# Optimization experiments

Measured on AMD Instinct MI355X. Metric: run time of the kernel, lower is better.

Reference implementation:

```python
import jax, jax.numpy as jnp
import numpy as np

BIG_NEG = -1000000000.0
B, N, X, D = 16, 32, 36, 2048
H = 512

def setup_inputs() -> dict:
    key = jax.random.key(0)
    ks = jax.random.split(key, 16)
    inp = {
        'fc_feats_target': jax.random.normal(ks[0], (B, 1, D), jnp.float32),
        'fc_feats_distr': jax.random.normal(ks[1], (B, N, D), jnp.float32),
        'att_feats_target': jax.random.normal(ks[2], (B, 1, X, D), jnp.float32),
        'att_feats_distr': jax.random.normal(ks[3], (B, N, X, D), jnp.float32),
        'att_masks_target': jax.random.randint(ks[4], (B, 1, X), 0, 2, jnp.int32),
        'att_masks_distr': jax.random.randint(ks[5], (B, N, X), 0, 2, jnp.int32),
        # scorer MLP params: Linear(2D->H), Linear(H->1)
        'W1': jax.random.normal(ks[6], (2 * D, H), jnp.float32) * 0.02,
        'b1': jnp.zeros((H,), jnp.float32),
        'W2': jax.random.normal(ks[7], (H, 1), jnp.float32) * 0.02,
        'b2': jnp.zeros((1,), jnp.float32),
        # bilinear weight, initialized to identity as in the module
        'Wbil': jnp.eye(D, dtype=jnp.float32),
        # object_scorer MLP params
        'oW1': jax.random.normal(ks[8], (2 * D, H), jnp.float32) * 0.02,
        'ob1': jnp.zeros((H,), jnp.float32),
        'oW2': jax.random.normal(ks[9], (H, 1), jnp.float32) * 0.02,
        'ob2': jnp.zeros((1,), jnp.float32),
    }
    return inp

def _mlp(x, W1, b1, W2, b2):
    h = jax.nn.relu(x @ W1 + b1)
    return (h @ W2 + b2)[..., 0]  # squeeze(-1)

def reference(fc_feats_target, fc_feats_distr, att_feats_target, att_feats_distr,
              att_masks_target, att_masks_distr,
              W1, b1, W2, b2, Wbil, oW1, ob1, oW2, ob2):
    # base scorer on global (fc) features
    ft = jnp.broadcast_to(fc_feats_target, fc_feats_distr.shape)  # [B,N,D]
    cat_feats = jnp.concatenate([ft, fc_feats_distr], axis=-1)    # [B,N,2D]
    scores = _mlp(cat_feats, W1, b1, W2, b2)                      # [B,N]

    # bilinear compatibility: einsum('bixd,biye,de->bixy') with target broadcast over i
    tproj = jnp.einsum('bxd,de->bxe', att_feats_target[:, 0], Wbil)        # [B,X,D]
    inners = jnp.einsum('bxd,biyd->bixy', tproj, att_feats_distr)          # [B,N,X,Y]

    mask_outer = (att_masks_target[:, 0][:, None, :, None]
                  * att_masks_distr[:, :, None, :])                        # [B,N,X,Y]
    inners = jnp.where(mask_outer > 0, inners, BIG_NEG)

    target_weights = jax.nn.softmax(jnp.max(inners, axis=3), axis=-1)      # [B,N,X]
    distr_weights = jax.nn.softmax(jnp.max(inners, axis=2), axis=-1)       # [B,N,Y]

    target_feats = jnp.einsum('bxd,bix->bid', att_feats_target[:, 0], target_weights)
    distr_feats = jnp.einsum('biyd,biy->bid', att_feats_distr, distr_weights)

    cat_att = jnp.concatenate([target_feats, distr_feats], axis=-1)        # [B,N,2D]
    scores = scores + _mlp(cat_att, oW1, ob1, oW2, ob2)

    return jax.nn.log_softmax(scores, axis=-1)  # [B,N]
```

## Files before the change

### kernel.cpp

```cpp
#include <hip/hip_runtime.h>
#include <math.h>

#define D_   2048
#define H_   512
#define K2D  4096
#define X_   36
#define NCOL 1152

#define Z_MLP 32
#define Z_TP  8

#define O_A   0u
#define O_B   9437184u
#define O_SB  11534336u
#define O_SO  11534848u
#define O_C   11536384u

typedef __attribute__((ext_vector_type(8))) short bf8_t;
typedef __attribute__((ext_vector_type(4))) float f4_t;

__device__ __forceinline__ unsigned short f2bf(float f) {
  unsigned u = __float_as_uint(f);
  unsigned r = u + 0x7FFFu + ((u >> 16) & 1u);
  return (unsigned short)(r >> 16);
}
__device__ __forceinline__ float bf2f(unsigned short h) {
  return __uint_as_float(((unsigned)h) << 16);
}

__device__ __forceinline__ void gload16(const void* g, void* l) {
  __builtin_amdgcn_global_load_lds(
      (const __attribute__((address_space(1))) unsigned int*)g,
      (__attribute__((address_space(3))) unsigned int*)l, 16, 0, 0);
}

#define TSTR 40

__device__ __forceinline__ void cvt8(unsigned short* Hp, unsigned short* Lp,
                                     float4 a, float4 b) {
  __align__(16) unsigned short h[8], l[8];
  float x[8] = {a.x, a.y, a.z, a.w, b.x, b.y, b.z, b.w};
  #pragma unroll
  for (int j = 0; j < 8; j++) {
    h[j] = f2bf(x[j]);
    l[j] = f2bf(x[j] - bf2f(h[j]));
  }
  *(bf8_t*)Hp = *(bf8_t*)&h[0];
  *(bf8_t*)Lp = *(bf8_t*)&l[0];
}

__device__ __forceinline__ void cvt8v(bf8_t* H, bf8_t* L, float4 a, float4 b) {
  float x[8] = {a.x, a.y, a.z, a.w, b.x, b.y, b.z, b.w};
  bf8_t hh, ll;
  #pragma unroll
  for (int j = 0; j < 8; j++) {
    unsigned short h = f2bf(x[j]);
    hh[j] = (short)h;
    ll[j] = (short)f2bf(x[j] - bf2f(h));
  }
  *H = hh; *L = ll;
}

__global__ __launch_bounds__(256, 4) void gemm_mfma64(
    const float* __restrict__ A, const float* __restrict__ A2,
    const float* __restrict__ Bm, float* __restrict__ Cpart,
    int M, int N, int K, int kchunk, int amode)
{
  __shared__ __align__(16) unsigned short AsH[64 * TSTR], AsL[64 * TSTR];
  __shared__ __align__(16) unsigned short BsH[64 * TSTR], BsL[64 * TSTR];
  const int t  = threadIdx.x;
  const int m0 = blockIdx.y << 6;
  const int n0 = blockIdx.x << 6;
  const int k0 = blockIdx.z * kchunk;
  const int kend = k0 + kchunk;
  const int w  = t >> 6;
  const int ln = t & 15;
  const int qd = (t >> 4) & 3;
  const int wm = (w >> 1) << 5;
  const int wn = (w & 1) << 5;
  const int a_row = t >> 2;
  const int a_kq  = (t & 3) << 3;
  const int b_col = t & 63;
  const int b_kq  = (t >> 6) << 3;

  f4_t acc[2][2];
  #pragma unroll
  for (int i = 0; i < 2; i++)
    #pragma unroll
    for (int j = 0; j < 2; j++) acc[i][j] = (f4_t)0.f;

  float4 pa0, pa1;
  float  pb[8];

  auto loadA = [&](int kb) {
    int gr = m0 + a_row;
    int gk = kb + a_kq;
    pa0 = make_float4(0.f, 0.f, 0.f, 0.f);
    pa1 = pa0;
    if (gr < M) {
      const float* src;
      if (amode == 0) src = A + (size_t)gr * K + gk;
      else src = (gk < 2048) ? (A  + ((size_t)(gr >> 5) << 11) + gk)
                             : (A2 + ((size_t)gr << 11) + (gk - 2048));
      pa0 = *(const float4*)src;
      pa1 = *(const float4*)(src + 4);
    }
  };
  auto loadB = [&](int kb) {
    #pragma unroll
    for (int j = 0; j < 8; j++)
      pb[j] = Bm[(size_t)(kb + b_kq + j) * N + n0 + b_col];
  };

  loadA(k0); loadB(k0);

  for (int kb = k0; kb < kend; kb += 32) {
    __syncthreads();
    cvt8(&AsH[a_row * TSTR + a_kq], &AsL[a_row * TSTR + a_kq], pa0, pa1);
    cvt8(&BsH[b_col * TSTR + b_kq], &BsL[b_col * TSTR + b_kq],
         make_float4(pb[0], pb[1], pb[2], pb[3]),
         make_float4(pb[4], pb[5], pb[6], pb[7]));
    __syncthreads();
    if (kb + 32 < kend) { loadA(kb + 32); loadB(kb + 32); }
    bf8_t ah[2], al[2], bh[2], bl[2];
    #pragma unroll
    for (int fm = 0; fm < 2; fm++) {
      int r = (wm + (fm << 4) + ln) * TSTR + (qd << 3);
      ah[fm] = *(const bf8_t*)&AsH[r];
      al[fm] = *(const bf8_t*)&AsL[r];
    }
    #pragma unroll
    for (int fn = 0; fn < 2; fn++) {
      int r = (wn + (fn << 4) + ln) * TSTR + (qd << 3);
      bh[fn] = *(const bf8_t*)&BsH[r];
      bl[fn] = *(const bf8_t*)&BsL[r];
    }
    #pragma unroll
    for (int fm = 0; fm < 2; fm++)
      #pragma unroll
      for (int fn = 0; fn < 2; fn++) {
        acc[fm][fn] = __builtin_amdgcn_mfma_f32_16x16x32_bf16(ah[fm], bh[fn], acc[fm][fn], 0, 0, 0);
        acc[fm][fn] = __builtin_amdgcn_mfma_f32_16x16x32_bf16(ah[fm], bl[fn], acc[fm][fn], 0, 0, 0);
        acc[fm][fn] = __builtin_amdgcn_mfma_f32_16x16x32_bf16(al[fm], bh[fn], acc[fm][fn], 0, 0, 0);
      }
  }
  float* Cz = Cpart + (size_t)blockIdx.z * M * N;
  #pragma unroll
  for (int fm = 0; fm < 2; fm++) {
    #pragma unroll
    for (int reg = 0; reg < 4; reg++) {
      int gr = m0 + wm + (fm << 4) + (qd << 2) + reg;
      if (gr < M) {
        #pragma unroll
        for (int fn = 0; fn < 2; fn++)
          Cz[(size_t)gr * N + n0 + wn + (fn << 4) + ln] = acc[fm][fn][reg];
      }
    }
  }
}

__global__ __launch_bounds__(256) void reduce_tp(
    const float* __restrict__ tpp, unsigned short* __restrict__ tH,
    unsigned short* __restrict__ tL)
{
  int idx = blockIdx.x * 256 + threadIdx.x;
  const float4* p = (const float4*)tpp;
  float4 a = p[idx];
  #pragma unroll
  for (int z = 1; z < Z_TP; z++) {
    float4 b = p[idx + (size_t)z * 294912];
    a.x += b.x; a.y += b.y; a.z += b.z; a.w += b.w;
  }
  ushort4 h, l;
  h.x = f2bf(a.x); l.x = f2bf(a.x - bf2f(h.x));
  h.y = f2bf(a.y); l.y = f2bf(a.y - bf2f(h.y));
  h.z = f2bf(a.z); l.z = f2bf(a.z - bf2f(h.z));
  h.w = f2bf(a.w); l.w = f2bf(a.w - bf2f(h.w));
  ((ushort4*)tH)[idx] = h;
  ((ushort4*)tL)[idx] = l;
}

__global__ __launch_bounds__(256) void mlp_tail_z(
    const float* __restrict__ hp, const float* __restrict__ b1,
    const float* __restrict__ w2, const float* __restrict__ b2,
    float* __restrict__ out)
{
  int row = blockIdx.x;
  int t   = threadIdx.x;
  float v = 0.f;
  #pragma unroll
  for (int q = 0; q < 2; q++) {
    int h = t + (q << 8);
    float s = 0.f;
    #pragma unroll
    for (int z = 0; z < Z_MLP; z++)
      s += hp[(size_t)z * (H_ * 512) + (size_t)row * H_ + h];
    s += b1[h];
    v += fmaxf(s, 0.f) * w2[h];
  }
  #pragma unroll
  for (int off = 32; off > 0; off >>= 1) v += __shfl_down(v, off, 64);
  __shared__ float red[4];
  if ((t & 63) == 0) red[t >> 6] = v;
  __syncthreads();
  if (t == 0) out[row] = red[0] + red[1] + red[2] + red[3] + b2[0];
}

__global__ __launch_bounds__(256, 2) void attn_bi(
    const unsigned short* __restrict__ tH,
    const float* __restrict__ attd,
    const int* __restrict__ amt, const int* __restrict__ amd,
    const float* __restrict__ attt, float* __restrict__ cat)
{
  __shared__ float Sp[4][36][37];
  __shared__ __align__(16) float Bs[4][2][1280];
  __shared__ int   mtv[36], mdv[36];
  __shared__ float mrow[36], mcol[36], twl[36], dwl[36];
  const int bi = blockIdx.x;
  const int b  = bi >> 5;
  const int t  = threadIdx.x;
  const int w  = t >> 6;
  const int lane = t & 63;
  const int ln = t & 15;
  const int qd = (t >> 4) & 3;
  if (t < 36) { mtv[t] = amt[b * 36 + t]; mdv[t] = amd[bi * 36 + t]; }

  const unsigned short* tLo = tH + 1179648;
  const int kw = w << 9;
  const unsigned short* AH[3];
  const unsigned short* AL[3];
  #pragma unroll
  for (int f = 0; f < 3; f++) {
    int r = f * 16 + ln; if (r > 35) r = 35;
    size_t ao = ((size_t)b * X_ + r) * D_ + kw + (qd << 3);
    AH[f] = tH  + ao;
    AL[f] = tLo + ao;
  }
  const float* Bbase = attd + (size_t)bi * X_ * D_;

  f4_t acc[3][3];
  #pragma unroll
  for (int i = 0; i < 3; i++)
    #pragma unroll
    for (int j = 0; j < 3; j++) acc[i][j] = (f4_t)0.f;

  auto stage = [&](int kk, int cc) {
    const int k0 = kw + (kk << 5);
    #pragma unroll
    for (int j = 0; j < 5; j++) {
      int r = j * 8 + (lane >> 3); if (r > 35) r = 35;
      int ss = (lane & 7) ^ (r & 7);
      gload16(Bbase + (size_t)r * D_ + k0 + (ss << 2), &Bs[w][cc][j << 8]);
    }
  };

  bf8_t ah[3], al[3];
  stage(0, 0);
  #pragma unroll
  for (int f = 0; f < 3; f++) {
    ah[f] = *(const bf8_t*)AH[f];
    al[f] = *(const bf8_t*)AL[f];
  }
  asm volatile("s_waitcnt vmcnt(0)" ::: "memory");
  __builtin_amdgcn_sched_barrier(0);

  int c = 0;
  for (int kk = 0; kk < 16; kk++) {
    if (kk < 15) stage(kk + 1, c ^ 1);
    bf8_t anH[3], anL[3];
    if (kk < 15) {
      const int o1 = (kk + 1) << 5;
      #pragma unroll
      for (int f = 0; f < 3; f++) {
        anH[f] = *(const bf8_t*)(AH[f] + o1);
        anL[f] = *(const bf8_t*)(AL[f] + o1);
      }
    }
    #pragma unroll
    for (int fn = 0; fn < 3; fn++) {
      int r = fn * 16 + ln; if (r > 35) r = 35;
      int base = r << 5;
      int s0 = (((qd << 1)    ) ^ (r & 7)) << 2;
      int s1 = (((qd << 1) | 1) ^ (r & 7)) << 2;
      float4 x0 = *(const float4*)&Bs[w][c][base + s0];
      float4 x1 = *(const float4*)&Bs[w][c][base + s1];
      bf8_t bh, bl;
      cvt8v(&bh, &bl, x0, x1);
      #pragma unroll
      for (int fm = 0; fm < 3; fm++) {
        acc[fm][fn] = __builtin_amdgcn_mfma_f32_16x16x32_bf16(ah[fm], bh, acc[fm][fn], 0, 0, 0);
        acc[fm][fn] = __builtin_amdgcn_mfma_f32_16x16x32_bf16(ah[fm], bl, acc[fm][fn], 0, 0, 0);
        acc[fm][fn] = __builtin_amdgcn_mfma_f32_16x16x32_bf16(al[fm], bh, acc[fm][fn], 0, 0, 0);
      }
    }
    asm volatile("s_waitcnt vmcnt(0)" ::: "memory");
    __builtin_amdgcn_sched_barrier(0);
    c ^= 1;
    if (kk < 15) {
      #pragma unroll
      for (int f = 0; f < 3; f++) { ah[f] = anH[f]; al[f] = anL[f]; }
    }
  }

  #pragma unroll
  for (int fm = 0; fm < 3; fm++)
    #pragma unroll
    for (int fn = 0; fn < 3; fn++)
      #pragma unroll
      for (int reg = 0; reg < 4; reg++) {
        int x = (fm << 4) + (qd << 2) + reg;
        int y = (fn << 4) + ln;
        if (x < 36 && y < 36) Sp[w][x][y] = acc[fm][fn][reg];
      }
  __syncthreads();
  for (int e = t; e < 1296; e += 256) {
    int x = e / 36, y = e - x * 36;
    float v = Sp[0][x][y] + Sp[1][x][y] + Sp[2][x][y] + Sp[3][x][y];
    Sp[0][x][y] = (mtv[x] != 0 && mdv[y] != 0) ? v : -1e9f;
  }
  __syncthreads();
  if (t < 36) {
    float r = -INFINITY, c2 = -INFINITY;
    for (int k = 0; k < 36; k++) {
      r  = fmaxf(r,  Sp[0][t][k]);
      c2 = fmaxf(c2, Sp[0][k][t]);
    }
    mrow[t] = r; mcol[t] = c2;
  }
  __syncthreads();
  if (t < 64) {
    float v = (t < 36) ? mrow[t] : -INFINITY;
    float m = v;
    #pragma unroll
    for (int off = 32; off > 0; off >>= 1) m = fmaxf(m, __shfl_xor(m, off, 64));
    float e = (t < 36) ? expf(v - m) : 0.f;
    float s = e;
    #pragma unroll
    for (int off = 32; off > 0; off >>= 1) s += __shfl_xor(s, off, 64);
    if (t < 36) twl[t] = e / s;
  } else if (t < 128) {
    int l = t - 64;
    float v = (l < 36) ? mcol[l] : -INFINITY;
    float m = v;
    #pragma unroll
    for (int off = 32; off > 0; off >>= 1) m = fmaxf(m, __shfl_xor(m, off, 64));
    float e = (l < 36) ? expf(v - m) : 0.f;
    float s = e;
    #pragma unroll
    for (int off = 32; off > 0; off >>= 1) s += __shfl_xor(s, off, 64);
    if (l < 36) dwl[l] = e / s;
  }
  __syncthreads();
  const float4* at4 = (const float4*)(attt + (size_t)b * X_ * D_);
  const float4* ad4 = (const float4*)(attd + (size_t)bi * X_ * D_);
  float4 t0 = make_float4(0, 0, 0, 0), t1 = t0, d0 = t0, d1 = t0;
  for (int x = 0; x < 36; x++) {
    float wt = twl[x], wd = dwl[x];
    float4 a  = at4[x * 512 + t];
    float4 a2 = at4[x * 512 + t + 256];
    float4 e  = ad4[x * 512 + t];
    float4 e2 = ad4[x * 512 + t + 256];
    t0.x = fmaf(wt, a.x, t0.x);  t0.y = fmaf(wt, a.y, t0.y);
    t0.z = fmaf(wt, a.z, t0.z);  t0.w = fmaf(wt, a.w, t0.w);
    t1.x = fmaf(wt, a2.x, t1.x); t1.y = fmaf(wt, a2.y, t1.y);
    t1.z = fmaf(wt, a2.z, t1.z); t1.w = fmaf(wt, a2.w, t1.w);
    d0.x = fmaf(wd, e.x, d0.x);  d0.y = fmaf(wd, e.y, d0.y);
    d0.z = fmaf(wd, e.z, d0.z);  d0.w = fmaf(wd, e.w, d0.w);
    d1.x = fmaf(wd, e2.x, d1.x); d1.y = fmaf(wd, e2.y, d1.y);
    d1.z = fmaf(wd, e2.z, d1.z); d1.w = fmaf(wd, e2.w, d1.w);
  }
  float4* c4 = (float4*)(cat + (size_t)bi * K2D);
  c4[t] = t0; c4[t + 256] = t1; c4[512 + t] = d0; c4[512 + t + 256] = d1;
}

__global__ __launch_bounds__(64) void lsm(
    const float* __restrict__ sb, const float* __restrict__ so,
    float* __restrict__ out)
{
  int b = blockIdx.x, t = threadIdx.x;
  float s = (t < 32) ? sb[b * 32 + t] + so[b * 32 + t] : -INFINITY;
  float m = s;
  #pragma unroll
  for (int off = 32; off > 0; off >>= 1) m = fmaxf(m, __shfl_xor(m, off, 64));
  float e = (t < 32) ? expf(s - m) : 0.f;
  float sum = e;
  #pragma unroll
  for (int off = 32; off > 0; off >>= 1) sum += __shfl_xor(sum, off, 64);
  if (t < 32) out[b * 32 + t] = s - m - logf(sum);
}

extern "C" void kernel_launch(void* const* d_in, const int* in_sizes, int n_in,
                              void* d_out, int out_size, void* d_ws, size_t ws_size,
                              hipStream_t stream)
{
  const float* fc_t  = (const float*)d_in[0];
  const float* fc_d  = (const float*)d_in[1];
  const float* att_t = (const float*)d_in[2];
  const float* att_d = (const float*)d_in[3];
  const int*   am_t  = (const int*)d_in[4];
  const int*   am_d  = (const int*)d_in[5];
  const float* W1    = (const float*)d_in[6];
  const float* b1    = (const float*)d_in[7];
  const float* W2    = (const float*)d_in[8];
  const float* b2    = (const float*)d_in[9];
  const float* Wbil  = (const float*)d_in[10];
  const float* oW1   = (const float*)d_in[11];
  const float* ob1   = (const float*)d_in[12];
  const float* oW2   = (const float*)d_in[13];
  const float* ob2   = (const float*)d_in[14];
  float* ws  = (float*)d_ws;
  float* out = (float*)d_out;

  gemm_mfma64<<<dim3(8, 8, Z_MLP), 256, 0, stream>>>(fc_t, fc_d, W1, ws + O_A,
                                                     512, 512, 4096, 4096 / Z_MLP, 1);
  mlp_tail_z<<<512, 256, 0, stream>>>(ws + O_A, b1, W2, b2, ws + O_SB);
  gemm_mfma64<<<dim3(32, 9, Z_TP), 256, 0, stream>>>(att_t, nullptr, Wbil, ws + O_A,
                                                     576, 2048, 2048, 2048 / Z_TP, 0);
  reduce_tp<<<1152, 256, 0, stream>>>(ws + O_A, (unsigned short*)(ws + O_B),
                                      (unsigned short*)(ws + O_B) + 1179648);
  attn_bi<<<512, 256, 0, stream>>>((const unsigned short*)(ws + O_B), att_d,
                                   am_t, am_d, att_t, ws + O_C);
  gemm_mfma64<<<dim3(8, 8, Z_MLP), 256, 0, stream>>>(ws + O_C, nullptr, oW1, ws + O_A,
                                                     512, 512, 4096, 4096 / Z_MLP, 0);
  mlp_tail_z<<<512, 256, 0, stream>>>(ws + O_A, ob1, oW2, ob2, ws + O_SO);
  lsm<<<16, 64, 0, stream>>>(ws + O_SB, ws + O_SO, out);
}
```

Baseline: 378.9 us.

## Stage shared 128-wide K chunks across all warps in attn_bi bilinear GEMM

Before, each of the four wavefronts staged its own contiguous 512-element K slice of the distractor features into a private LDS buffer. Now the block cooperatively loads 128-column K chunks covering all 36 rows into one shared double buffer, with each wave owning a 32-column sub-slice, and uses a 32-way XOR swizzle. The aim is longer contiguous global reads per row (512 bytes instead of 128) for better coalescing. In exchange it adds a __syncthreads per iteration in place of the wave-local schedule barrier, which serialises the waves.

```diff
diff --git a/kernel.cpp b/kernel.cpp
--- a/kernel.cpp
+++ b/kernel.cpp
@@ -213,7 +213,7 @@
     const float* __restrict__ attt, float* __restrict__ cat)
 {
   __shared__ float Sp[4][36][37];
-  __shared__ __align__(16) float Bs[4][2][1280];
+  __shared__ __align__(16) float Bs[2][36 * 128];
   __shared__ int   mtv[36], mdv[36];
   __shared__ float mrow[36], mcol[36], twl[36], dwl[36];
   const int bi = blockIdx.x;
@@ -226,13 +226,12 @@
   if (t < 36) { mtv[t] = amt[b * 36 + t]; mdv[t] = amd[bi * 36 + t]; }
 
   const unsigned short* tLo = tH + 1179648;
-  const int kw = w << 9;
   const unsigned short* AH[3];
   const unsigned short* AL[3];
   #pragma unroll
   for (int f = 0; f < 3; f++) {
     int r = f * 16 + ln; if (r > 35) r = 35;
-    size_t ao = ((size_t)b * X_ + r) * D_ + kw + (qd << 3);
+    size_t ao = ((size_t)b * X_ + r) * D_ + (w << 5) + (qd << 3);
     AH[f] = tH  + ao;
     AL[f] = tLo + ao;
   }
@@ -244,13 +243,19 @@
     #pragma unroll
     for (int j = 0; j < 3; j++) acc[i][j] = (f4_t)0.f;
 
-  auto stage = [&](int kk, int cc) {
-    const int k0 = kw + (kk << 5);
+  const int g0 = (w < 2) ? w * 5 : 10 + (w - 2) * 4;
+  const int gn = (w < 2) ? 5 : 4;
+  auto stage = [&](int sc, int cc) {
     #pragma unroll
     for (int j = 0; j < 5; j++) {
-      int r = j * 8 + (lane >> 3); if (r > 35) r = 35;
-      int ss = (lane & 7) ^ (r & 7);
-      gload16(Bbase + (size_t)r * D_ + k0 + (ss << 2), &Bs[w][cc][j << 8]);
+      if (j < gn) {
+        int g = g0 + j;
+        int r = (g << 1) + (lane >> 5);
+        int p = lane & 31;
+        int s = p ^ (r & 31);
+        gload16(Bbase + (size_t)r * D_ + (sc << 7) + (s << 2),
+                &Bs[cc][g << 8]);
+      }
     }
   };
 
@@ -262,14 +267,14 @@
     al[f] = *(const bf8_t*)AL[f];
   }
   asm volatile("s_waitcnt vmcnt(0)" ::: "memory");
-  __builtin_amdgcn_sched_barrier(0);
+  __syncthreads();
 
   int c = 0;
-  for (int kk = 0; kk < 16; kk++) {
-    if (kk < 15) stage(kk + 1, c ^ 1);
+  for (int sc = 0; sc < 16; sc++) {
+    if (sc < 15) stage(sc + 1, c ^ 1);
     bf8_t anH[3], anL[3];
-    if (kk < 15) {
-      const int o1 = (kk + 1) << 5;
+    if (sc < 15) {
+      const int o1 = (sc + 1) << 7;
       #pragma unroll
       for (int f = 0; f < 3; f++) {
         anH[f] = *(const bf8_t*)(AH[f] + o1);
@@ -279,11 +284,11 @@
     #pragma unroll
     for (int fn = 0; fn < 3; fn++) {
       int r = fn * 16 + ln; if (r > 35) r = 35;
-      int base = r << 5;
-      int s0 = (((qd << 1)    ) ^ (r & 7)) << 2;
-      int s1 = (((qd << 1) | 1) ^ (r & 7)) << 2;
-      float4 x0 = *(const float4*)&Bs[w][c][base + s0];
-      float4 x1 = *(const float4*)&Bs[w][c][base + s1];
+      int s0 = (w << 3) | (qd << 1);
+      int p0 = s0 ^ (r & 31);
+      int p1 = (s0 | 1) ^ (r & 31);
+      const float4 x0 = *(const float4*)&Bs[c][((r << 5) + p0) << 2];
+      const float4 x1 = *(const float4*)&Bs[c][((r << 5) + p1) << 2];
       bf8_t bh, bl;
       cvt8v(&bh, &bl, x0, x1);
       #pragma unroll
@@ -294,9 +299,9 @@
       }
     }
     asm volatile("s_waitcnt vmcnt(0)" ::: "memory");
-    __builtin_amdgcn_sched_barrier(0);
+    __syncthreads();
     c ^= 1;
-    if (kk < 15) {
+    if (sc < 15) {
       #pragma unroll
       for (int f = 0; f < 3; f++) { ah[f] = anH[f]; al[f] = anL[f]; }
     }
```

After: 373.4 us. Within noise of the previous version (-1.5%).
